# Kernel tuning notes

Measured on AMD Instinct MI355X. Metric: run time of the kernel, lower is better.

Reference implementation:

```python
import jax, jax.numpy as jnp
import numpy as np

B, S, H = 8, 4096, 1152
LENGTH = 256


def setup_inputs() -> dict:
    key = jax.random.key(0)
    k1, k2 = jax.random.split(key)
    hidden_states = jax.random.normal(k1, (B, S, H), dtype=jnp.float32)
    # (x, y) patch coordinates on a 64x64 grid
    patch_positions = jax.random.randint(k2, (B, S, 2), 0, 64, dtype=jnp.int64)
    padding_positions = jnp.ones((B, LENGTH), dtype=jnp.bool_)
    return {
        "hidden_states": hidden_states,
        "patch_positions": patch_positions,
        "padding_positions": padding_positions,
    }


def _pool(hidden_states, patch_positions, length):
    b, s, h = hidden_states.shape
    k = int((s // length) ** 0.5)
    k_sq = k * k
    assert k_sq * length == s
    clamped = jnp.maximum(patch_positions, 0)  # clamp(min=0)
    max_x = jnp.max(clamped[..., 0], axis=-1, keepdims=True) + 1  # [B,1]
    kidx = clamped // k
    kernel_idxs = kidx[..., 0] + (max_x // k) * kidx[..., 1]  # [B,S], values < length
    # segment-mean instead of the one-hot GEMM: identical math
    seg = (kernel_idxs + length * jnp.arange(b, dtype=kernel_idxs.dtype)[:, None]).reshape(-1)
    pooled = jax.ops.segment_sum(
        hidden_states.reshape(b * s, h), seg, num_segments=b * length
    ).reshape(b, length, h) / k_sq
    counts = jax.ops.segment_sum(
        jnp.ones((b * s,), dtype=jnp.int32), seg, num_segments=b * length
    ).reshape(b, length)
    mask = counts > 0  # equivalent to ~(weights == 0).all(dim=1)
    return pooled, mask


def reference(hidden_states, patch_positions, padding_positions):
    length = LENGTH
    if hidden_states.shape[1] == length:
        pooled, mask = hidden_states, padding_positions
    else:
        pooled, mask = _pool(hidden_states, patch_positions, length)
    root_hidden_size = float(hidden_states.shape[-1]) ** 0.5
    pooled = pooled * root_hidden_size
    return pooled, mask
```

## Files before the change

kernel.cpp:

```cpp
#include <hip/hip_runtime.h>
#include <hip/hip_bf16.h>

#define NB 8
#define NS 4096
#define NH 1152
#define LEN 256
#define NT 576

typedef float vf2 __attribute__((ext_vector_type(2)));

__global__ __launch_bounds__(NT) void gvp_fused(
        const float* __restrict__ hidden,
        const int* __restrict__ patch,
        float* __restrict__ out,
        float* __restrict__ maskout) {
    int g = blockIdx.x;
    int b = g >> 8;
    int myseg = g & (LEN - 1);
    int t = threadIdx.x;

    __shared__ int rows[NS];
    __shared__ int s_max[9];
    __shared__ int s_cnt, s_mult;
    if (t == 0) s_cnt = 0;

    const int2* p2 = (const int2*)(patch + (size_t)b * NS * 2);
    int pk[8];
    int m = 0;
    #pragma unroll
    for (int i = 0; i < 7; ++i) {
        int2 v = p2[t + NT * i];
        int x = v.x < 0 ? 0 : v.x;
        int y = v.y < 0 ? 0 : v.y;
        pk[i] = x | (y << 16);
        m = max(m, x);
    }
    pk[7] = -1;
    if (t < NS - NT * 7) {
        int2 v = p2[t + NT * 7];
        int x = v.x < 0 ? 0 : v.x;
        int y = v.y < 0 ? 0 : v.y;
        pk[7] = x | (y << 16);
        m = max(m, x);
    }
    #pragma unroll
    for (int off = 32; off > 0; off >>= 1)
        m = max(m, __shfl_down(m, off, 64));
    if ((t & 63) == 0) s_max[t >> 6] = m;
    __syncthreads();
    if (t == 0) {
        int mm = s_max[0];
        #pragma unroll
        for (int j = 1; j < 9; ++j) mm = max(mm, s_max[j]);
        s_mult = (mm + 1) >> 2;
    }
    __syncthreads();
    int mult = s_mult;

    #pragma unroll
    for (int i = 0; i < 8; ++i) {
        if (pk[i] >= 0) {
            int x = pk[i] & 0xffff, y = pk[i] >> 16;
            int seg = (x >> 2) + mult * (y >> 2);
            if (seg == myseg)
                rows[atomicAdd(&s_cnt, 1)] = t + NT * i;
        }
    }
    __syncthreads();
    int cnt = s_cnt;

    const float* hb = hidden + (size_t)b * NS * NH;
    vf2 a0 = 0.f, a1 = 0.f;
    int r = 0;
    for (; r + 7 < cnt; r += 8) {
        vf2 v0 = ((const vf2*)(hb + (size_t)rows[r + 0] * NH))[t];
        vf2 v1 = ((const vf2*)(hb + (size_t)rows[r + 1] * NH))[t];
        vf2 v2 = ((const vf2*)(hb + (size_t)rows[r + 2] * NH))[t];
        vf2 v3 = ((const vf2*)(hb + (size_t)rows[r + 3] * NH))[t];
        vf2 v4 = ((const vf2*)(hb + (size_t)rows[r + 4] * NH))[t];
        vf2 v5 = ((const vf2*)(hb + (size_t)rows[r + 5] * NH))[t];
        vf2 v6 = ((const vf2*)(hb + (size_t)rows[r + 6] * NH))[t];
        vf2 v7 = ((const vf2*)(hb + (size_t)rows[r + 7] * NH))[t];
        v0 += v1; v2 += v3; v4 += v5; v6 += v7;
        v0 += v2; v4 += v6;
        a0 += v0; a1 += v4;
    }
    for (; r < cnt; ++r)
        a0 += ((const vf2*)(hb + (size_t)rows[r] * NH))[t];
    a0 += a1;

    const float scale = 2.1213203435596424f;
    ((vf2*)(out + (size_t)g * NH))[t] = a0 * scale;
    if (t == 0) maskout[g] = (cnt > 0) ? 1.0f : 0.0f;
}

extern "C" void kernel_launch(void* const* d_in, const int* in_sizes, int n_in,
                              void* d_out, int out_size, void* d_ws, size_t ws_size,
                              hipStream_t stream) {
    const float* hidden = (const float*)d_in[0];
    const int*   patch  = (const int*)d_in[1];
    float* out = (float*)d_out;
    float* maskout = out + (size_t)NB * LEN * NH;

    gvp_fused<<<NB * LEN, NT, 0, stream>>>(hidden, patch, out, maskout);
}
```

Measured before the change: 35.80 us.

## Process four segments per block with 1024 threads and float4 gathers

Each block now handles four consecutive segments of one batch instead of one, so the patch-position scan and bucketing are amortized across four outputs. Rows are bucketed with per-segment counts, an offset prefix and a scatter pass. Each 256-thread sub-group gathers its segment's rows with 16-byte float4 loads. The leftover 128 columns (1152 = 256*4 + 128) are covered by a separate strided pass reduced through shared memory, which adds extra syncs and shared traffic and runs with fewer blocks (512).

```diff
diff --git a/kernel.cpp b/kernel.cpp
--- a/kernel.cpp
+++ b/kernel.cpp
@@ -5,42 +5,39 @@
 #define NS 4096
 #define NH 1152
 #define LEN 256
-#define NT 576
+#define NT 1024
+#define SEGS 4
 
-typedef float vf2 __attribute__((ext_vector_type(2)));
+typedef float vf4 __attribute__((ext_vector_type(4)));
 
 __global__ __launch_bounds__(NT) void gvp_fused(
         const float* __restrict__ hidden,
         const int* __restrict__ patch,
         float* __restrict__ out,
         float* __restrict__ maskout) {
-    int g = blockIdx.x;
-    int b = g >> 8;
-    int myseg = g & (LEN - 1);
+    int gq = blockIdx.x;
+    int b = gq >> 6;
+    int seg0 = (gq & 63) * SEGS;
     int t = threadIdx.x;
+    int sub = t >> 8;
+    int tl = t & 255;
 
-    __shared__ int rows[NS];
-    __shared__ int s_max[9];
-    __shared__ int s_cnt, s_mult;
-    if (t == 0) s_cnt = 0;
+    __shared__ __align__(16) int rows[NS];
+    __shared__ vf4 s_red[NT];
+    __shared__ int s_max[16];
+    __shared__ int s_cnt[SEGS], s_off[SEGS], s_cur[SEGS];
+    __shared__ int s_mult;
+    if (t < SEGS) s_cnt[t] = 0;
 
     const int2* p2 = (const int2*)(patch + (size_t)b * NS * 2);
-    int pk[8];
+    int pk[4];
     int m = 0;
     #pragma unroll
-    for (int i = 0; i < 7; ++i) {
+    for (int i = 0; i < 4; ++i) {
         int2 v = p2[t + NT * i];
         int x = v.x < 0 ? 0 : v.x;
         int y = v.y < 0 ? 0 : v.y;
         pk[i] = x | (y << 16);
-        m = max(m, x);
-    }
-    pk[7] = -1;
-    if (t < NS - NT * 7) {
-        int2 v = p2[t + NT * 7];
-        int x = v.x < 0 ? 0 : v.x;
-        int y = v.y < 0 ? 0 : v.y;
-        pk[7] = x | (y << 16);
         m = max(m, x);
     }
     #pragma unroll
@@ -51,47 +48,78 @@
     if (t == 0) {
         int mm = s_max[0];
         #pragma unroll
-        for (int j = 1; j < 9; ++j) mm = max(mm, s_max[j]);
+        for (int j = 1; j < 16; ++j) mm = max(mm, s_max[j]);
         s_mult = (mm + 1) >> 2;
     }
     __syncthreads();
     int mult = s_mult;
 
     #pragma unroll
-    for (int i = 0; i < 8; ++i) {
-        if (pk[i] >= 0) {
-            int x = pk[i] & 0xffff, y = pk[i] >> 16;
-            int seg = (x >> 2) + mult * (y >> 2);
-            if (seg == myseg)
-                rows[atomicAdd(&s_cnt, 1)] = t + NT * i;
-        }
+    for (int i = 0; i < 4; ++i) {
+        int x = pk[i] & 0xffff, y = pk[i] >> 16;
+        int d = (x >> 2) + mult * (y >> 2) - seg0;
+        if ((unsigned)d < SEGS) atomicAdd(&s_cnt[d], 1);
     }
     __syncthreads();
-    int cnt = s_cnt;
+    if (t == 0) {
+        int o = 0;
+        #pragma unroll
+        for (int d = 0; d < SEGS; ++d) { s_off[d] = o; s_cur[d] = o; o += s_cnt[d]; }
+    }
+    __syncthreads();
+    #pragma unroll
+    for (int i = 0; i < 4; ++i) {
+        int x = pk[i] & 0xffff, y = pk[i] >> 16;
+        int d = (x >> 2) + mult * (y >> 2) - seg0;
+        if ((unsigned)d < SEGS)
+            rows[atomicAdd(&s_cur[d], 1)] = t + NT * i;
+    }
+    __syncthreads();
+
+    int cnt = s_cnt[sub];
+    const int* myrows = rows + s_off[sub];
 
     const float* hb = hidden + (size_t)b * NS * NH;
-    vf2 a0 = 0.f, a1 = 0.f;
+    vf4 a0 = 0.f, a1 = 0.f;
     int r = 0;
     for (; r + 7 < cnt; r += 8) {
-        vf2 v0 = ((const vf2*)(hb + (size_t)rows[r + 0] * NH))[t];
-        vf2 v1 = ((const vf2*)(hb + (size_t)rows[r + 1] * NH))[t];
-        vf2 v2 = ((const vf2*)(hb + (size_t)rows[r + 2] * NH))[t];
-        vf2 v3 = ((const vf2*)(hb + (size_t)rows[r + 3] * NH))[t];
-        vf2 v4 = ((const vf2*)(hb + (size_t)rows[r + 4] * NH))[t];
-        vf2 v5 = ((const vf2*)(hb + (size_t)rows[r + 5] * NH))[t];
-        vf2 v6 = ((const vf2*)(hb + (size_t)rows[r + 6] * NH))[t];
-        vf2 v7 = ((const vf2*)(hb + (size_t)rows[r + 7] * NH))[t];
+        const vf4* p0 = (const vf4*)(hb + (size_t)myrows[r + 0] * NH);
+        const vf4* p1 = (const vf4*)(hb + (size_t)myrows[r + 1] * NH);
+        const vf4* p2r = (const vf4*)(hb + (size_t)myrows[r + 2] * NH);
+        const vf4* p3 = (const vf4*)(hb + (size_t)myrows[r + 3] * NH);
+        const vf4* p4 = (const vf4*)(hb + (size_t)myrows[r + 4] * NH);
+        const vf4* p5 = (const vf4*)(hb + (size_t)myrows[r + 5] * NH);
+        const vf4* p6 = (const vf4*)(hb + (size_t)myrows[r + 6] * NH);
+        const vf4* p7 = (const vf4*)(hb + (size_t)myrows[r + 7] * NH);
+        vf4 v0 = p0[tl], v1 = p1[tl], v2 = p2r[tl], v3 = p3[tl];
+        vf4 v4 = p4[tl], v5 = p5[tl], v6 = p6[tl], v7 = p7[tl];
         v0 += v1; v2 += v3; v4 += v5; v6 += v7;
         v0 += v2; v4 += v6;
         a0 += v0; a1 += v4;
     }
     for (; r < cnt; ++r)
-        a0 += ((const vf2*)(hb + (size_t)rows[r] * NH))[t];
+        a0 += ((const vf4*)(hb + (size_t)myrows[r] * NH))[tl];
     a0 += a1;
 
+    int l = tl & 31;
+    int grp = tl >> 5;
+    vf4 a2 = 0.f;
+    for (int r2 = grp; r2 < cnt; r2 += 8)
+        a2 += ((const vf4*)(hb + (size_t)myrows[r2] * NH))[256 + l];
+    s_red[t] = a2;
+    __syncthreads();
+
     const float scale = 2.1213203435596424f;
-    ((vf2*)(out + (size_t)g * NH))[t] = a0 * scale;
-    if (t == 0) maskout[g] = (cnt > 0) ? 1.0f : 0.0f;
+    int g = (b << 8) + seg0 + sub;
+    vf4* og = (vf4*)(out + (size_t)g * NH);
+    og[tl] = a0 * scale;
+    if (tl < 32) {
+        vf4 s = 0.f;
+        #pragma unroll
+        for (int j = 0; j < 8; ++j) s += s_red[(sub << 8) + j * 32 + tl];
+        og[256 + tl] = s * scale;
+    }
+    if (tl == 0) maskout[g] = (cnt > 0) ? 1.0f : 0.0f;
 }
 
 extern "C" void kernel_launch(void* const* d_in, const int* in_sizes, int n_in,
@@ -102,5 +130,5 @@
     float* out = (float*)d_out;
     float* maskout = out + (size_t)NB * LEN * NH;
 
-    gvp_fused<<<NB * LEN, NT, 0, stream>>>(hidden, patch, out, maskout);
+    gvp_fused<<<NB * LEN / SEGS, NT, 0, stream>>>(hidden, patch, out, maskout);
 }
```

Result: faster. 31.87 us (-11.0%).
